# Kernel optimization log

Hardware: AMD Instinct MI355X
Metric: run time of the kernel (lower is better)

Reference implementation:

```python
import jax, jax.numpy as jnp
import numpy as np

C = 64
G = 4
K = 3
GC = C // G
OS = 1.0  # offset_scale
OM_DIM = int(np.ceil(G * K * K * 3 / 8) * 8)  # 112, padded; only first G*27 used


def setup_inputs() -> dict:
    key = jax.random.key(0)
    ks = jax.random.split(key, 8)
    B, H, W = 2, 384, 384
    s = 0.02
    return {
        "inp": jax.random.normal(ks[0], (B, C, H, W), jnp.float32),
        "Wv": jax.random.normal(ks[1], (C, C), jnp.float32) * s,
        "bv": jnp.zeros((C,), jnp.float32),
        "Wdw": jax.random.normal(ks[2], (C, 1, K, K), jnp.float32) * s,
        "bdw": jnp.zeros((C,), jnp.float32),
        "Wom": jax.random.normal(ks[3], (C, OM_DIM), jnp.float32) * s,
        "bom": jnp.zeros((OM_DIM,), jnp.float32),
        "Wo": jax.random.normal(ks[4], (C, C), jnp.float32) * s,
    }


def _bilinear(v, px, py, H, W, b_idx, g_idx):
    # v: (B,H,W,G,GC); px,py: (B,H,W,G) pixel coords; zero padding outside.
    x0 = jnp.floor(px)
    y0 = jnp.floor(py)
    wx1 = px - x0
    wy1 = py - y0
    x0i = x0.astype(jnp.int32)
    y0i = y0.astype(jnp.int32)
    out = jnp.zeros(px.shape + (v.shape[-1],), v.dtype)
    for dy, wy in ((0, 1.0 - wy1), (1, wy1)):
        for dx, wx in ((0, 1.0 - wx1), (1, wx1)):
            xi = x0i + dx
            yi = y0i + dy
            valid = ((xi >= 0) & (xi < W) & (yi >= 0) & (yi < H)).astype(v.dtype)
            xc = jnp.clip(xi, 0, W - 1)
            yc = jnp.clip(yi, 0, H - 1)
            g = v[b_idx, yc, xc, g_idx]  # (B,H,W,G,GC)
            out = out + g * (wy * wx * valid)[..., None]
    return out


def reference(inp, Wv, bv, Wdw, bdw, Wom, bom, Wo):
    B, _, H, W = inp.shape
    x = inp.transpose(0, 2, 3, 1)  # (B,H,W,C)
    # value projection, split into groups
    value = (x @ Wv + bv).reshape(B, H, W, G, GC)
    # depthwise conv on input feeds the offset/mask predictor
    dw = jax.lax.conv_general_dilated(
        inp, Wdw, window_strides=(1, 1), padding=[(1, 1), (1, 1)],
        feature_group_count=C) + bdw[None, :, None, None]
    om = dw.transpose(0, 2, 3, 1) @ Wom + bom  # (B,H,W,OM_DIM)
    om = om[..., : G * K * K * 3].reshape(B, H, W, G, K * K * 3)
    off = om[..., : K * K * 2].reshape(B, H, W, G, K * K, 2)  # (dx,dy) per point
    mask = om[..., K * K * 2:]  # (B,H,W,G,K*K), no softmax in DCNv4

    base_x = jnp.arange(W, dtype=value.dtype)[None, None, :, None]
    base_y = jnp.arange(H, dtype=value.dtype)[None, :, None, None]
    b_idx = jnp.arange(B)[:, None, None, None]
    g_idx = jnp.arange(G)[None, None, None, :]

    out = jnp.zeros((B, H, W, G, GC), value.dtype)
    k = 0
    for ky in range(K):
        for kx in range(K):
            dx = off[..., k, 0]
            dy = off[..., k, 1]
            px = base_x + ((kx - K // 2) + dx) * OS
            py = base_y + ((ky - K // 2) + dy) * OS
            samp = _bilinear(value, px, py, H, W, b_idx, g_idx)
            out = out + samp * mask[..., k][..., None]
            k += 1

    out = out.reshape(B, H, W, C) @ Wo  # output_proj, no bias (output_bias=False)
    return out.transpose(0, 3, 1, 2)  # back to (B,C,H,W)
```

## Files before the change

kernel.cpp:

```cpp
#include <hip/hip_runtime.h>
#include <hip/hip_bf16.h>
#include <math.h>

namespace {
constexpr int kH = 384, kW = 384, kBn = 2;
constexpr int kHW = kH * kW;
constexpr int kOMD = 112;
constexpr int kNB = kBn * (kHW / 64);
constexpr int kNB8 = kNB / 8;
}

__device__ __forceinline__ int swz(int bid) {
    return (bid & 7) * kNB8 + (bid >> 3);
}

__device__ __forceinline__ void fma4(float* acc, float a, float4 w) {
    acc[0] = fmaf(a, w.x, acc[0]);
    acc[1] = fmaf(a, w.y, acc[1]);
    acc[2] = fmaf(a, w.z, acc[2]);
    acc[3] = fmaf(a, w.w, acc[3]);
}

__device__ __forceinline__ float bl(unsigned u) {
    return __uint_as_float(u << 16);
}
__device__ __forceinline__ float bh(unsigned u) {
    return __uint_as_float(u & 0xffff0000u);
}
__device__ __forceinline__ unsigned short f2bf(float f) {
    union { __hip_bfloat16 b; unsigned short s; } u;
    u.b = __float2bfloat16(f);
    return u.s;
}

__global__ __launch_bounds__(256) void k_value(
        const float* __restrict__ inp, const float* __restrict__ Wv,
        const float* __restrict__ bv, unsigned short* __restrict__ value) {
    __shared__ float xin[64][64];
    const int tid = threadIdx.x;
    const int bid = swz(blockIdx.x);
    const int b = bid / (kHW / 64);
    const int pix0 = (bid % (kHW / 64)) * 64;
    const float* ib = inp + (size_t)b * 64 * kHW + pix0;
    for (int i = tid; i < 1024; i += 256) {
        const int c = i >> 4, p4 = (i & 15) << 2;
        const float4 v = *(const float4*)(ib + (size_t)c * kHW + p4);
        *(float4*)&xin[c][p4] = v;
    }
    __syncthreads();

    const int p = tid & 63;
    const int g = __builtin_amdgcn_readfirstlane(tid >> 6);

    float acc[16];
    {
        const float* bg = bv + g * 16;
        #pragma unroll
        for (int j = 0; j < 16; ++j) acc[j] = bg[j];
    }
    #pragma unroll 4
    for (int ci = 0; ci < 64; ++ci) {
        const float a = xin[ci][p];
        const float* wr = Wv + ci * 64 + g * 16;
        #pragma unroll
        for (int j = 0; j < 16; ++j) acc[j] = fmaf(a, wr[j], acc[j]);
    }

    unsigned u[8];
    #pragma unroll
    for (int j = 0; j < 8; ++j)
        u[j] = (unsigned)f2bf(acc[2 * j]) | ((unsigned)f2bf(acc[2 * j + 1]) << 16);
    uint4* vo = (uint4*)(value + ((size_t)(b * 4 + g) * kHW + pix0 + p) * 16);
    vo[0] = make_uint4(u[0], u[1], u[2], u[3]);
    vo[1] = make_uint4(u[4], u[5], u[6], u[7]);
}

__global__ __launch_bounds__(256) void k_main(
        const float* __restrict__ inp, const float* __restrict__ Wdw,
        const float* __restrict__ bdw, const float* __restrict__ Wom,
        const float* __restrict__ bom, const float* __restrict__ Wo,
        const unsigned short* __restrict__ value, float* __restrict__ out) {
    __shared__ float lds1[64][68];

    const int tid = threadIdx.x;
    const int bid = swz(blockIdx.x);
    const int b = bid / (kH * (kW / 64));
    const int rem = bid % (kH * (kW / 64));
    const int h = rem / (kW / 64);
    const int w0 = (rem % (kW / 64)) * 64;

    const int p = tid & 63;
    const int g = tid >> 6;
    const int gs = __builtin_amdgcn_readfirstlane(g);

    {
        const int w = w0 + p;
        #pragma unroll 4
        for (int cc = 0; cc < 16; ++cc) {
            const int c = gs * 16 + cc;
            const float* ib = inp + (size_t)(b * 64 + c) * kHW;
            float s = bdw[c];
            #pragma unroll
            for (int r = 0; r < 3; ++r) {
                const int y = h - 1 + r;
                if (y >= 0 && y < kH) {
                    const float* rowp = ib + (size_t)y * kW;
                    #pragma unroll
                    for (int kx = 0; kx < 3; ++kx) {
                        const int x = w - 1 + kx;
                        const float v = (x >= 0 && x < kW) ? rowp[x] : 0.f;
                        s = fmaf(v, Wdw[c * 9 + r * 3 + kx], s);
                    }
                }
            }
            lds1[c][p] = s;
        }
    }
    __syncthreads();

    float om[27];
    {
        const float* bg = bom + gs * 27;
        #pragma unroll
        for (int j = 0; j < 27; ++j) om[j] = bg[j];
        #pragma unroll 4
        for (int ci = 0; ci < 64; ++ci) {
            const float a = lds1[ci][p];
            const float* wr = Wom + ci * kOMD + gs * 27;
            #pragma unroll
            for (int j = 0; j < 27; ++j) om[j] = fmaf(a, wr[j], om[j]);
        }
    }
    __syncthreads();

    {
        float acc[16];
        #pragma unroll
        for (int j = 0; j < 16; ++j) acc[j] = 0.f;
        const float fw = (float)(w0 + p);
        const float fh = (float)h;
        const unsigned short* vbase = value + (size_t)(b * 4 + gs) * kHW * 16;
        #pragma unroll
        for (int k = 0; k < 9; ++k) {
            const int ky = k / 3, kx = k % 3;
            const float dx = om[2 * k];
            const float dy = om[2 * k + 1];
            const float m = om[18 + k];
            const float px = fw + (float)(kx - 1) + dx;
            const float py = fh + (float)(ky - 1) + dy;
            const float x0f = floorf(px), y0f = floorf(py);
            const int x0 = (int)x0f, y0 = (int)y0f;
            const float wx1 = px - x0f, wy1 = py - y0f;
            const float wx0 = 1.f - wx1, wy0 = 1.f - wy1;
            #pragma unroll
            for (int cor = 0; cor < 4; ++cor) {
                const int dy2 = cor >> 1, dx2 = cor & 1;
                const int xi = x0 + dx2, yi = y0 + dy2;
                float wgt = (dy2 ? wy1 : wy0) * (dx2 ? wx1 : wx0) * m;
                if (xi < 0 || xi >= kW || yi < 0 || yi >= kH) wgt = 0.f;
                const int xc = min(max(xi, 0), kW - 1);
                const int yc = min(max(yi, 0), kH - 1);
                const uint4* vp = (const uint4*)(vbase +
                        ((size_t)yc * kW + xc) * 16);
                const uint4 u0 = vp[0];
                const uint4 u1 = vp[1];
                acc[0]  = fmaf(wgt, bl(u0.x), acc[0]);
                acc[1]  = fmaf(wgt, bh(u0.x), acc[1]);
                acc[2]  = fmaf(wgt, bl(u0.y), acc[2]);
                acc[3]  = fmaf(wgt, bh(u0.y), acc[3]);
                acc[4]  = fmaf(wgt, bl(u0.z), acc[4]);
                acc[5]  = fmaf(wgt, bh(u0.z), acc[5]);
                acc[6]  = fmaf(wgt, bl(u0.w), acc[6]);
                acc[7]  = fmaf(wgt, bh(u0.w), acc[7]);
                acc[8]  = fmaf(wgt, bl(u1.x), acc[8]);
                acc[9]  = fmaf(wgt, bh(u1.x), acc[9]);
                acc[10] = fmaf(wgt, bl(u1.y), acc[10]);
                acc[11] = fmaf(wgt, bh(u1.y), acc[11]);
                acc[12] = fmaf(wgt, bl(u1.z), acc[12]);
                acc[13] = fmaf(wgt, bh(u1.z), acc[13]);
                acc[14] = fmaf(wgt, bl(u1.w), acc[14]);
                acc[15] = fmaf(wgt, bh(u1.w), acc[15]);
            }
        }
        #pragma unroll
        for (int j = 0; j < 16; ++j) lds1[gs * 16 + j][p] = acc[j];
    }
    __syncthreads();

    {
        const int cg = gs;
        float acc[16];
        #pragma unroll
        for (int j = 0; j < 16; ++j) acc[j] = 0.f;
        #pragma unroll 4
        for (int ci = 0; ci < 64; ++ci) {
            const float a = lds1[ci][p];
            const float* wr = Wo + ci * 64 + cg * 16;
            #pragma unroll
            for (int j = 0; j < 16; ++j) acc[j] = fmaf(a, wr[j], acc[j]);
        }
        float* ob = out + (size_t)(b * 64 + cg * 16) * kHW + (size_t)h * kW + w0 + p;
        #pragma unroll
        for (int j = 0; j < 16; ++j) ob[(size_t)j * kHW] = acc[j];
    }
}

extern "C" void kernel_launch(void* const* d_in, const int* in_sizes, int n_in,
                              void* d_out, int out_size, void* d_ws, size_t ws_size,
                              hipStream_t stream) {
    const float* inp = (const float*)d_in[0];
    const float* Wv  = (const float*)d_in[1];
    const float* bv  = (const float*)d_in[2];
    const float* Wdw = (const float*)d_in[3];
    const float* bdw = (const float*)d_in[4];
    const float* Wom = (const float*)d_in[5];
    const float* bom = (const float*)d_in[6];
    const float* Wo  = (const float*)d_in[7];
    float* outp = (float*)d_out;
    unsigned short* value = (unsigned short*)d_ws;

    k_value<<<kNB, 256, 0, stream>>>(inp, Wv, bv, value);
    k_main<<<kNB, 256, 0, stream>>>(inp, Wdw, bdw, Wom, bom, Wo, value, outp);
}
```

Before: 332.5 us.

## Fuse value and main kernels into persistent cooperative kernel with grid sync

Merges the value-projection and sampling kernels into a single persistent cooperative kernel of 1536 blocks that loop over tiles, with a grid-wide barrier between the two phases. This removes the second kernel launch and the tail gap between kernels. It also switches value storage from bf16 to fp16 for better precision. The risks are the cost of the grid sync, lost occupancy from the fixed grid with launch bounds of 6, and a fallback to two launches if the cooperative launch fails.

Result: slower. 729.3 us (+119.4%).

```diff
diff --git a/kernel.cpp b/kernel.cpp
--- a/kernel.cpp
+++ b/kernel.cpp
@@ -1,6 +1,9 @@
 #include <hip/hip_runtime.h>
-#include <hip/hip_bf16.h>
+#include <hip/hip_fp16.h>
+#include <hip/hip_cooperative_groups.h>
 #include <math.h>
+
+namespace cg = cooperative_groups;
 
 namespace {
 constexpr int kH = 384, kW = 384, kBn = 2;
@@ -8,201 +11,220 @@
 constexpr int kOMD = 112;
 constexpr int kNB = kBn * (kHW / 64);
 constexpr int kNB8 = kNB / 8;
-}
-
-__device__ __forceinline__ int swz(int bid) {
-    return (bid & 7) * kNB8 + (bid >> 3);
-}
-
-__device__ __forceinline__ void fma4(float* acc, float a, float4 w) {
-    acc[0] = fmaf(a, w.x, acc[0]);
-    acc[1] = fmaf(a, w.y, acc[1]);
-    acc[2] = fmaf(a, w.z, acc[2]);
-    acc[3] = fmaf(a, w.w, acc[3]);
-}
-
-__device__ __forceinline__ float bl(unsigned u) {
-    return __uint_as_float(u << 16);
-}
-__device__ __forceinline__ float bh(unsigned u) {
-    return __uint_as_float(u & 0xffff0000u);
-}
-__device__ __forceinline__ unsigned short f2bf(float f) {
-    union { __hip_bfloat16 b; unsigned short s; } u;
-    u.b = __float2bfloat16(f);
-    return u.s;
-}
-
-__global__ __launch_bounds__(256) void k_value(
+constexpr int kGrid = 1536;
+}
+
+__device__ __forceinline__ int swz(int t) {
+    return (t & 7) * kNB8 + (t >> 3);
+}
+
+__device__ __forceinline__ unsigned pack2h(float a, float b) {
+    unsigned short lo = __builtin_bit_cast(unsigned short, __float2half_rn(a));
+    unsigned short hi = __builtin_bit_cast(unsigned short, __float2half_rn(b));
+    return (unsigned)lo | ((unsigned)hi << 16);
+}
+
+__device__ __forceinline__ void fma2h(float& a0, float& a1, float w, unsigned u) {
+    __half2 h = __builtin_bit_cast(__half2, u);
+    a0 = fmaf(w, __half2float(h.x), a0);
+    a1 = fmaf(w, __half2float(h.y), a1);
+}
+
+__device__ __forceinline__ void phase_value(
+        const float* __restrict__ inp, const float* __restrict__ Wv,
+        const float* __restrict__ bv, unsigned short* __restrict__ value,
+        float (*lds1)[68]) {
+    const int tid = threadIdx.x;
+    const int p = tid & 63;
+    const int gs = __builtin_amdgcn_readfirstlane(tid >> 6);
+
+    for (int t = blockIdx.x; t < kNB; t += gridDim.x) {
+        const int bid = swz(t);
+        const int b = bid / (kHW / 64);
+        const int pix0 = (bid % (kHW / 64)) * 64;
+        const float* ib = inp + (size_t)b * 64 * kHW + pix0;
+
+        __syncthreads();
+        for (int i = tid; i < 1024; i += 256) {
+            const int c = i >> 4, p4 = (i & 15) << 2;
+            const float4 v = *(const float4*)(ib + (size_t)c * kHW + p4);
+            *(float4*)&lds1[c][p4] = v;
+        }
+        __syncthreads();
+
+        float acc[16];
+        {
+            const float* bg = bv + gs * 16;
+            #pragma unroll
+            for (int j = 0; j < 16; ++j) acc[j] = bg[j];
+        }
+        #pragma unroll 4
+        for (int ci = 0; ci < 64; ++ci) {
+            const float a = lds1[ci][p];
+            const float* wr = Wv + ci * 64 + gs * 16;
+            #pragma unroll
+            for (int j = 0; j < 16; ++j) acc[j] = fmaf(a, wr[j], acc[j]);
+        }
+
+        unsigned u[8];
+        #pragma unroll
+        for (int j = 0; j < 8; ++j) u[j] = pack2h(acc[2 * j], acc[2 * j + 1]);
+        uint4* vo = (uint4*)(value + ((size_t)(b * 4 + gs) * kHW + pix0 + p) * 16);
+        vo[0] = make_uint4(u[0], u[1], u[2], u[3]);
+        vo[1] = make_uint4(u[4], u[5], u[6], u[7]);
+    }
+}
+
+__device__ __forceinline__ void phase_main(
+        const float* __restrict__ inp, const float* __restrict__ Wdw,
+        const float* __restrict__ bdw, const float* __restrict__ Wom,
+        const float* __restrict__ bom, const float* __restrict__ Wo,
+        const unsigned short* __restrict__ value, float* __restrict__ out,
+        float (*lds1)[68]) {
+    const int tid = threadIdx.x;
+    const int p = tid & 63;
+    const int gs = __builtin_amdgcn_readfirstlane(tid >> 6);
+
+    for (int t = blockIdx.x; t < kNB; t += gridDim.x) {
+        const int bid = swz(t);
+        const int b = bid / (kH * (kW / 64));
+        const int rem = bid % (kH * (kW / 64));
+        const int h = rem / (kW / 64);
+        const int w0 = (rem % (kW / 64)) * 64;
+
+        __syncthreads();
+
+        {
+            const int w = w0 + p;
+            #pragma unroll 4
+            for (int cc = 0; cc < 16; ++cc) {
+                const int c = gs * 16 + cc;
+                const float* ib = inp + (size_t)(b * 64 + c) * kHW;
+                float s = bdw[c];
+                #pragma unroll
+                for (int r = 0; r < 3; ++r) {
+                    const int y = h - 1 + r;
+                    if (y >= 0 && y < kH) {
+                        const float* rowp = ib + (size_t)y * kW;
+                        #pragma unroll
+                        for (int kx = 0; kx < 3; ++kx) {
+                            const int x = w - 1 + kx;
+                            const float v = (x >= 0 && x < kW) ? rowp[x] : 0.f;
+                            s = fmaf(v, Wdw[c * 9 + r * 3 + kx], s);
+                        }
+                    }
+                }
+                lds1[c][p] = s;
+            }
+        }
+        __syncthreads();
+
+        float om[27];
+        {
+            const float* bg = bom + gs * 27;
+            #pragma unroll
+            for (int j = 0; j < 27; ++j) om[j] = bg[j];
+            #pragma unroll 4
+            for (int ci = 0; ci < 64; ++ci) {
+                const float a = lds1[ci][p];
+                const float* wr = Wom + ci * kOMD + gs * 27;
+                #pragma unroll
+                for (int j = 0; j < 27; ++j) om[j] = fmaf(a, wr[j], om[j]);
+            }
+        }
+        __syncthreads();
+
+        {
+            float acc[16];
+            #pragma unroll
+            for (int j = 0; j < 16; ++j) acc[j] = 0.f;
+            const float fw = (float)(w0 + p);
+            const float fh = (float)h;
+            const unsigned short* vbase = value + (size_t)(b * 4 + gs) * kHW * 16;
+            #pragma unroll
+            for (int k = 0; k < 9; ++k) {
+                const int ky = k / 3, kx = k % 3;
+                const float dx = om[2 * k];
+                const float dy = om[2 * k + 1];
+                const float m = om[18 + k];
+                const float px = fw + (float)(kx - 1) + dx;
+                const float py = fh + (float)(ky - 1) + dy;
+                const float x0f = floorf(px), y0f = floorf(py);
+                const int x0 = (int)x0f, y0 = (int)y0f;
+                const float wx1 = px - x0f, wy1 = py - y0f;
+                const float wx0 = 1.f - wx1, wy0 = 1.f - wy1;
+                #pragma unroll
+                for (int cor = 0; cor < 4; ++cor) {
+                    const int dy2 = cor >> 1, dx2 = cor & 1;
+                    const int xi = x0 + dx2, yi = y0 + dy2;
+                    float wgt = (dy2 ? wy1 : wy0) * (dx2 ? wx1 : wx0) * m;
+                    if (xi < 0 || xi >= kW || yi < 0 || yi >= kH) wgt = 0.f;
+                    const int xc = min(max(xi, 0), kW - 1);
+                    const int yc = min(max(yi, 0), kH - 1);
+                    const uint4* vp = (const uint4*)(vbase +
+                            ((size_t)yc * kW + xc) * 16);
+                    const uint4 u0 = vp[0];
+                    const uint4 u1 = vp[1];
+                    fma2h(acc[0],  acc[1],  wgt, u0.x);
+                    fma2h(acc[2],  acc[3],  wgt, u0.y);
+                    fma2h(acc[4],  acc[5],  wgt, u0.z);
+                    fma2h(acc[6],  acc[7],  wgt, u0.w);
+                    fma2h(acc[8],  acc[9],  wgt, u1.x);
+                    fma2h(acc[10], acc[11], wgt, u1.y);
+                    fma2h(acc[12], acc[13], wgt, u1.z);
+                    fma2h(acc[14], acc[15], wgt, u1.w);
+                }
+            }
+            #pragma unroll
+            for (int j = 0; j < 16; ++j) lds1[gs * 16 + j][p] = acc[j];
+        }
+        __syncthreads();
+
+        {
+            float acc[16];
+            #pragma unroll
+            for (int j = 0; j < 16; ++j) acc[j] = 0.f;
+            #pragma unroll 4
+            for (int ci = 0; ci < 64; ++ci) {
+                const float a = lds1[ci][p];
+                const float* wr = Wo + ci * 64 + gs * 16;
+                #pragma unroll
+                for (int j = 0; j < 16; ++j) acc[j] = fmaf(a, wr[j], acc[j]);
+            }
+            float* ob = out + (size_t)(b * 64 + gs * 16) * kHW + (size_t)h * kW + w0 + p;
+            #pragma unroll
+            for (int j = 0; j < 16; ++j) ob[(size_t)j * kHW] = acc[j];
+        }
+    }
+}
+
+__global__ __launch_bounds__(256, 6) void k_fused(
+        const float* __restrict__ inp, const float* __restrict__ Wv,
+        const float* __restrict__ bv, const float* __restrict__ Wdw,
+        const float* __restrict__ bdw, const float* __restrict__ Wom,
+        const float* __restrict__ bom, const float* __restrict__ Wo,
+        unsigned short* __restrict__ value, float* __restrict__ out) {
+    __shared__ float lds1[64][68];
+    phase_value(inp, Wv, bv, value, lds1);
+    __threadfence();
+    cg::this_grid().sync();
+    phase_main(inp, Wdw, bdw, Wom, bom, Wo, value, out, lds1);
+}
+
+__global__ __launch_bounds__(256) void k_p1(
         const float* __restrict__ inp, const float* __restrict__ Wv,
         const float* __restrict__ bv, unsigned short* __restrict__ value) {
-    __shared__ float xin[64][64];
-    const int tid = threadIdx.x;
-    const int bid = swz(blockIdx.x);
-    const int b = bid / (kHW / 64);
-    const int pix0 = (bid % (kHW / 64)) * 64;
-    const float* ib = inp + (size_t)b * 64 * kHW + pix0;
-    for (int i = tid; i < 1024; i += 256) {
-        const int c = i >> 4, p4 = (i & 15) << 2;
-        const float4 v = *(const float4*)(ib + (size_t)c * kHW + p4);
-        *(float4*)&xin[c][p4] = v;
-    }
-    __syncthreads();
-
-    const int p = tid & 63;
-    const int g = __builtin_amdgcn_readfirstlane(tid >> 6);
-
-    float acc[16];
-    {
-        const float* bg = bv + g * 16;
-        #pragma unroll
-        for (int j = 0; j < 16; ++j) acc[j] = bg[j];
-    }
-    #pragma unroll 4
-    for (int ci = 0; ci < 64; ++ci) {
-        const float a = xin[ci][p];
-        const float* wr = Wv + ci * 64 + g * 16;
-        #pragma unroll
-        for (int j = 0; j < 16; ++j) acc[j] = fmaf(a, wr[j], acc[j]);
-    }
-
-    unsigned u[8];
-    #pragma unroll
-    for (int j = 0; j < 8; ++j)
-        u[j] = (unsigned)f2bf(acc[2 * j]) | ((unsigned)f2bf(acc[2 * j + 1]) << 16);
-    uint4* vo = (uint4*)(value + ((size_t)(b * 4 + g) * kHW + pix0 + p) * 16);
-    vo[0] = make_uint4(u[0], u[1], u[2], u[3]);
-    vo[1] = make_uint4(u[4], u[5], u[6], u[7]);
-}
-
-__global__ __launch_bounds__(256) void k_main(
+    __shared__ float lds1[64][68];
+    phase_value(inp, Wv, bv, value, lds1);
+}
+
+__global__ __launch_bounds__(256) void k_p2(
         const float* __restrict__ inp, const float* __restrict__ Wdw,
         const float* __restrict__ bdw, const float* __restrict__ Wom,
         const float* __restrict__ bom, const float* __restrict__ Wo,
         const unsigned short* __restrict__ value, float* __restrict__ out) {
     __shared__ float lds1[64][68];
-
-    const int tid = threadIdx.x;
-    const int bid = swz(blockIdx.x);
-    const int b = bid / (kH * (kW / 64));
-    const int rem = bid % (kH * (kW / 64));
-    const int h = rem / (kW / 64);
-    const int w0 = (rem % (kW / 64)) * 64;
-
-    const int p = tid & 63;
-    const int g = tid >> 6;
-    const int gs = __builtin_amdgcn_readfirstlane(g);
-
-    {
-        const int w = w0 + p;
-        #pragma unroll 4
-        for (int cc = 0; cc < 16; ++cc) {
-            const int c = gs * 16 + cc;
-            const float* ib = inp + (size_t)(b * 64 + c) * kHW;
-            float s = bdw[c];
-            #pragma unroll
-            for (int r = 0; r < 3; ++r) {
-                const int y = h - 1 + r;
-                if (y >= 0 && y < kH) {
-                    const float* rowp = ib + (size_t)y * kW;
-                    #pragma unroll
-                    for (int kx = 0; kx < 3; ++kx) {
-                        const int x = w - 1 + kx;
-                        const float v = (x >= 0 && x < kW) ? rowp[x] : 0.f;
-                        s = fmaf(v, Wdw[c * 9 + r * 3 + kx], s);
-                    }
-                }
-            }
-            lds1[c][p] = s;
-        }
-    }
-    __syncthreads();
-
-    float om[27];
-    {
-        const float* bg = bom + gs * 27;
-        #pragma unroll
-        for (int j = 0; j < 27; ++j) om[j] = bg[j];
-        #pragma unroll 4
-        for (int ci = 0; ci < 64; ++ci) {
-            const float a = lds1[ci][p];
-            const float* wr = Wom + ci * kOMD + gs * 27;
-            #pragma unroll
-            for (int j = 0; j < 27; ++j) om[j] = fmaf(a, wr[j], om[j]);
-        }
-    }
-    __syncthreads();
-
-    {
-        float acc[16];
-        #pragma unroll
-        for (int j = 0; j < 16; ++j) acc[j] = 0.f;
-        const float fw = (float)(w0 + p);
-        const float fh = (float)h;
-        const unsigned short* vbase = value + (size_t)(b * 4 + gs) * kHW * 16;
-        #pragma unroll
-        for (int k = 0; k < 9; ++k) {
-            const int ky = k / 3, kx = k % 3;
-            const float dx = om[2 * k];
-            const float dy = om[2 * k + 1];
-            const float m = om[18 + k];
-            const float px = fw + (float)(kx - 1) + dx;
-            const float py = fh + (float)(ky - 1) + dy;
-            const float x0f = floorf(px), y0f = floorf(py);
-            const int x0 = (int)x0f, y0 = (int)y0f;
-            const float wx1 = px - x0f, wy1 = py - y0f;
-            const float wx0 = 1.f - wx1, wy0 = 1.f - wy1;
-            #pragma unroll
-            for (int cor = 0; cor < 4; ++cor) {
-                const int dy2 = cor >> 1, dx2 = cor & 1;
-                const int xi = x0 + dx2, yi = y0 + dy2;
-                float wgt = (dy2 ? wy1 : wy0) * (dx2 ? wx1 : wx0) * m;
-                if (xi < 0 || xi >= kW || yi < 0 || yi >= kH) wgt = 0.f;
-                const int xc = min(max(xi, 0), kW - 1);
-                const int yc = min(max(yi, 0), kH - 1);
-                const uint4* vp = (const uint4*)(vbase +
-                        ((size_t)yc * kW + xc) * 16);
-                const uint4 u0 = vp[0];
-                const uint4 u1 = vp[1];
-                acc[0]  = fmaf(wgt, bl(u0.x), acc[0]);
-                acc[1]  = fmaf(wgt, bh(u0.x), acc[1]);
-                acc[2]  = fmaf(wgt, bl(u0.y), acc[2]);
-                acc[3]  = fmaf(wgt, bh(u0.y), acc[3]);
-                acc[4]  = fmaf(wgt, bl(u0.z), acc[4]);
-                acc[5]  = fmaf(wgt, bh(u0.z), acc[5]);
-                acc[6]  = fmaf(wgt, bl(u0.w), acc[6]);
-                acc[7]  = fmaf(wgt, bh(u0.w), acc[7]);
-                acc[8]  = fmaf(wgt, bl(u1.x), acc[8]);
-                acc[9]  = fmaf(wgt, bh(u1.x), acc[9]);
-                acc[10] = fmaf(wgt, bl(u1.y), acc[10]);
-                acc[11] = fmaf(wgt, bh(u1.y), acc[11]);
-                acc[12] = fmaf(wgt, bl(u1.z), acc[12]);
-                acc[13] = fmaf(wgt, bh(u1.z), acc[13]);
-                acc[14] = fmaf(wgt, bl(u1.w), acc[14]);
-                acc[15] = fmaf(wgt, bh(u1.w), acc[15]);
-            }
-        }
-        #pragma unroll
-        for (int j = 0; j < 16; ++j) lds1[gs * 16 + j][p] = acc[j];
-    }
-    __syncthreads();
-
-    {
-        const int cg = gs;
-        float acc[16];
-        #pragma unroll
-        for (int j = 0; j < 16; ++j) acc[j] = 0.f;
-        #pragma unroll 4
-        for (int ci = 0; ci < 64; ++ci) {
-            const float a = lds1[ci][p];
-            const float* wr = Wo + ci * 64 + cg * 16;
-            #pragma unroll
-            for (int j = 0; j < 16; ++j) acc[j] = fmaf(a, wr[j], acc[j]);
-        }
-        float* ob = out + (size_t)(b * 64 + cg * 16) * kHW + (size_t)h * kW + w0 + p;
-        #pragma unroll
-        for (int j = 0; j < 16; ++j) ob[(size_t)j * kHW] = acc[j];
-    }
+    phase_main(inp, Wdw, bdw, Wom, bom, Wo, value, out, lds1);
 }
 
 extern "C" void kernel_launch(void* const* d_in, const int* in_sizes, int n_in,
@@ -219,6 +241,12 @@
     float* outp = (float*)d_out;
     unsigned short* value = (unsigned short*)d_ws;
 
-    k_value<<<kNB, 256, 0, stream>>>(inp, Wv, bv, value);
-    k_main<<<kNB, 256, 0, stream>>>(inp, Wdw, bdw, Wom, bom, Wo, value, outp);
-}
+    void* args[] = {(void*)&inp, (void*)&Wv, (void*)&bv, (void*)&Wdw, (void*)&bdw,
+                    (void*)&Wom, (void*)&bom, (void*)&Wo, (void*)&value, (void*)&outp};
+    hipError_t err = hipLaunchCooperativeKernel((void*)k_fused, dim3(kGrid), dim3(256),
+                                                args, 0, stream);
+    if (err != hipSuccess) {
+        k_p1<<<kNB, 256, 0, stream>>>(inp, Wv, bv, value);
+        k_p2<<<kNB, 256, 0, stream>>>(inp, Wdw, bdw, Wom, bom, Wo, value, outp);
+    }
+}
```
